# Performance work log

Measured on AMD Instinct MI355X. Metric: run time of the kernel, lower is better.

The kernel has to match this reference:

```python
import jax, jax.numpy as jnp
import numpy as np

N = 50000      # nodes
E = 800000     # edges (avg degree 16)
IN = 128       # in_feats
HID = 32       # hidden_feats per head
H = 4          # num_heads
NEG_SLOPE = 0.2


def setup_inputs() -> dict:
    key = jax.random.key(0)
    ks = jax.random.split(key, 13)
    x = jax.random.normal(ks[0], (N, IN), jnp.float32)
    src = jax.random.randint(ks[1], (E,), 0, N, jnp.int32)
    dst = jax.random.randint(ks[2], (E,), 0, N, jnp.int32)

    def lin(k, fi, fo):
        return jax.random.normal(k, (fi, fo), jnp.float32) * (1.0 / np.sqrt(fi))

    # conv1: IN -> H*HID
    W1 = lin(ks[3], IN, H * HID)
    al1 = jax.random.normal(ks[4], (H, HID), jnp.float32) * 0.1
    ar1 = jax.random.normal(ks[5], (H, HID), jnp.float32) * 0.1
    b1 = jnp.zeros((H, HID), jnp.float32)
    # conv2: H*HID -> H*HID
    W2 = lin(ks[6], H * HID, H * HID)
    al2 = jax.random.normal(ks[7], (H, HID), jnp.float32) * 0.1
    ar2 = jax.random.normal(ks[8], (H, HID), jnp.float32) * 0.1
    b2 = jnp.zeros((H, HID), jnp.float32)
    # fc: HID -> 1
    fcW = lin(ks[9], HID, 1)
    fcb = jnp.zeros((1,), jnp.float32)
    return {"x": x, "src": src, "dst": dst,
            "W1": W1, "al1": al1, "ar1": ar1, "b1": b1,
            "W2": W2, "al2": al2, "ar2": ar2, "b2": b2,
            "fcW": fcW, "fcb": fcb}


def gat_conv(x, src, dst, W, al, ar, b):
    # x: [N, F_in] -> feat: [N, H, HID]
    feat = (x @ W).reshape(N, H, HID)
    el = jnp.sum(feat * al, axis=-1)            # [N, H]
    er = jnp.sum(feat * ar, axis=-1)            # [N, H]
    e = jax.nn.leaky_relu(el[src] + er[dst], NEG_SLOPE)  # [E, H]
    # segment softmax over incoming edges of each dst node
    m = jax.ops.segment_max(e, dst, num_segments=N)      # [N, H]
    ex = jnp.exp(e - m[dst])                              # [E, H]
    denom = jax.ops.segment_sum(ex, dst, num_segments=N)  # [N, H]
    alpha = ex / denom[dst]                                # [E, H]
    msg = feat[src] * alpha[:, :, None]                    # [E, H, HID]
    out = jax.ops.segment_sum(msg, dst, num_segments=N)   # [N, H, HID]
    return out + b[None, :, :]


def reference(x, src, dst, W1, al1, ar1, b1, W2, al2, ar2, b2, fcW, fcb):
    h = gat_conv(x, src, dst, W1, al1, ar1, b1).reshape(N, H * HID)
    h = jax.nn.relu(h)
    # dropout(0.5) is identity in eval mode
    h = gat_conv(h, src, dst, W2, al2, ar2, b2).mean(axis=1)  # [N, HID]
    return h @ fcW + fcb                                       # [N, 1]
```

## Files before the change

### kernel.cpp

```cpp
#include <hip/hip_runtime.h>
#include <hip/hip_fp16.h>

#define LEAK 0.2f
#define CAP 64
#define CS 16

static __device__ inline int swz(int c, int j) {
    int qb = j >> 3, r = j & 7;
    return c * 144 + qb * 8 + (qb >> 2) * 4 + r;
}
static __device__ inline unsigned q4(float4 v, float is) {
    int x0 = __float2int_rn(v.x * is) + 128; x0 = min(max(x0, 0), 255);
    int x1 = __float2int_rn(v.y * is) + 128; x1 = min(max(x1, 0), 255);
    int x2 = __float2int_rn(v.z * is) + 128; x2 = min(max(x2, 0), 255);
    int x3 = __float2int_rn(v.w * is) + 128; x3 = min(max(x3, 0), 255);
    return (unsigned)x0 | ((unsigned)x1 << 8) | ((unsigned)x2 << 16) | ((unsigned)x3 << 24);
}

__global__ __launch_bounds__(256) void k0(
    int* __restrict__ cnt,
    const float* __restrict__ W2, const float* __restrict__ al2,
    const float* __restrict__ ar2, const float* __restrict__ fcW,
    const float* __restrict__ b2, float* __restrict__ WfT,
    float* __restrict__ bc, int N, int zb) {
    const int b = blockIdx.x;
    const int t = threadIdx.x;
    if (b < zb) {
        int i = b * 256 + t;
        if (i < N * (CS / 4)) ((int4*)cnt)[i] = make_int4(0, 0, 0, 0);
        return;
    }
    int idx = (b - zb) * 256 + t;
    if (idx < 1536) {
        int c = idx >> 7, k = idx & 127;
        int h = c & 3, sel = c >> 2;
        const float* vec = (sel == 0) ? (al2 + 32 * h)
                         : (sel == 1) ? (ar2 + 32 * h) : fcW;
        float s = 0.f;
#pragma unroll 8
        for (int m = 0; m < 32; m++) s += W2[k * 128 + 32 * h + m] * vec[m];
        WfT[c * 128 + k] = s;
    } else if (idx < 1540) {
        int h = idx - 1536;
        float s = 0.f;
        for (int m = 0; m < 32; m++) s += b2[h * 32 + m] * fcW[m];
        bc[h] = s;
    }
}

__global__ __launch_bounds__(256, 4) void k1f(
    const float* __restrict__ X, const float* __restrict__ W,
    const float* __restrict__ al, const float* __restrict__ ar,
    float2* __restrict__ elsc2, float* __restrict__ er_nh,
    unsigned* __restrict__ fq8,
    const int* __restrict__ src, const int* __restrict__ dst,
    int* __restrict__ cnt, unsigned short* __restrict__ ell,
    int N, int E, int gtiles, int R) {
    __shared__ float sW[32 * 128];
    __shared__ float sXT[32 * 64];
    const int b = blockIdx.x;
    const int t = threadIdx.x;

    if (b >= gtiles) {
        const int bb = b - gtiles;
        const int part = bb & 7;
        const int rank = bb >> 3;
        const int S = (N + 7) >> 3;
        const int lo = part * S;
        const int hi = (lo + S < N) ? (lo + S) : N;
        const int per = (E + R - 1) / R;
        const int e0 = rank * per;
        const int e1 = (e0 + per < E) ? (e0 + per) : E;
        for (int e = e0 + t; e < e1; e += 256) {
            int d = dst[e];
            if (d >= lo && d < hi) {
                int s = src[e];
                int pos = atomicAdd(&cnt[d * CS], 1);
                if (pos < CAP) ell[(size_t)d * CAP + pos] = (unsigned short)s;
            }
        }
        return;
    }

    const int r0 = b * 64;
    const int tx = t & 15;
    const int ty = t >> 4;
    const float4* X4 = (const float4*)X;
    const float4* W4 = (const float4*)W;
    float4* sW4 = (float4*)sW;
    const float4* sXT4 = (const float4*)sXT;

    float4 acc[4][2];
#pragma unroll
    for (int r = 0; r < 4; r++) {
        acc[r][0] = make_float4(0.f, 0.f, 0.f, 0.f);
        acc[r][1] = make_float4(0.f, 0.f, 0.f, 0.f);
    }
    for (int ks = 0; ks < 4; ++ks) {
        if (ks) __syncthreads();
#pragma unroll
        for (int i = 0; i < 4; i++) {
            int idx = i * 256 + t;
            sW4[idx] = W4[1024 * ks + idx];
        }
#pragma unroll
        for (int i = 0; i < 2; i++) {
            int idx = i * 256 + t;
            int row = idx >> 3;
            int kq = idx & 7;
            float4 v = make_float4(0.f, 0.f, 0.f, 0.f);
            if (r0 + row < N) v = X4[(size_t)(r0 + row) * 32 + ks * 8 + kq];
            int sc = ((row >> 2) ^ kq) * 4 + (row & 3);
            sXT[(4 * kq + 0) * 64 + sc] = v.x;
            sXT[(4 * kq + 1) * 64 + sc] = v.y;
            sXT[(4 * kq + 2) * 64 + sc] = v.z;
            sXT[(4 * kq + 3) * 64 + sc] = v.w;
        }
        __syncthreads();
#pragma unroll 4
        for (int k = 0; k < 32; k++) {
            float4 w0 = sW4[k * 32 + tx];
            float4 w1 = sW4[k * 32 + 16 + tx];
            float4 x0 = sXT4[k * 16 + (ty ^ (k >> 2))];
            float xs[4] = {x0.x, x0.y, x0.z, x0.w};
#pragma unroll
            for (int r = 0; r < 4; r++) {
                acc[r][0].x += xs[r] * w0.x; acc[r][0].y += xs[r] * w0.y;
                acc[r][0].z += xs[r] * w0.z; acc[r][0].w += xs[r] * w0.w;
                acc[r][1].x += xs[r] * w1.x; acc[r][1].y += xs[r] * w1.y;
                acc[r][1].z += xs[r] * w1.z; acc[r][1].w += xs[r] * w1.w;
            }
        }
    }
    const float4* al4p = (const float4*)al;
    const float4* ar4p = (const float4*)ar;
    float4 alA = al4p[tx], alB = al4p[16 + tx];
    float4 arA = ar4p[tx], arB = ar4p[16 + tx];
#pragma unroll
    for (int r = 0; r < 4; r++) {
        int row = r0 + ty * 4 + r;
        bool ok = row < N;
        float4 a0 = acc[r][0], a1 = acc[r][1];
        float m = fmaxf(fmaxf(fmaxf(fabsf(a0.x), fabsf(a0.y)),
                              fmaxf(fabsf(a0.z), fabsf(a0.w))),
                        fmaxf(fmaxf(fabsf(a1.x), fabsf(a1.y)),
                              fmaxf(fabsf(a1.z), fabsf(a1.w))));
#pragma unroll
        for (int off = 1; off < 16; off <<= 1) m = fmaxf(m, __shfl_xor(m, off));
        float scale = m * (1.f / 127.f);
        float is = (m > 0.f) ? (127.f / m) : 0.f;
        if (ok) {
            fq8[(size_t)row * 32 + tx] = q4(a0, is);
            fq8[(size_t)row * 32 + 16 + tx] = q4(a1, is);
        }
        float elA = a0.x * alA.x + a0.y * alA.y + a0.z * alA.z + a0.w * alA.w;
        float erA = a0.x * arA.x + a0.y * arA.y + a0.z * arA.z + a0.w * arA.w;
        float elB = a1.x * alB.x + a1.y * alB.y + a1.z * alB.z + a1.w * alB.w;
        float erB = a1.x * arB.x + a1.y * arB.y + a1.z * arB.z + a1.w * arB.w;
#pragma unroll
        for (int off = 1; off < 8; off <<= 1) {
            elA += __shfl_xor(elA, off); erA += __shfl_xor(erA, off);
            elB += __shfl_xor(elB, off); erB += __shfl_xor(erB, off);
        }
        if (ok && tx == 0) {
            elsc2[row * 4 + 0] = make_float2(elA, scale);
            elsc2[row * 4 + 2] = make_float2(elB, scale);
            er_nh[row * 4 + 0] = erA;
            er_nh[row * 4 + 2] = erB;
        }
        if (ok && tx == 8) {
            elsc2[row * 4 + 1] = make_float2(elA, scale);
            elsc2[row * 4 + 3] = make_float2(elB, scale);
            er_nh[row * 4 + 1] = erA;
            er_nh[row * 4 + 3] = erB;
        }
    }
}

__global__ __launch_bounds__(256) void k_agg1P(
    const unsigned* __restrict__ fq8, const float2* __restrict__ elsc2,
    const float* __restrict__ er_nh, const unsigned short* __restrict__ ell,
    const int* __restrict__ cnt, const float* __restrict__ b1,
    const float* __restrict__ WfT, float2* __restrict__ Pag,
    float* __restrict__ er2, int N) {
    __shared__ float sWf[12 * 144];
    for (int i = threadIdx.x; i < 1536; i += 256)
        sWf[swz(i >> 7, i & 127)] = WfT[i];
    __syncthreads();
    const int wave = threadIdx.x >> 6, lane = threadIdx.x & 63;
    const int nsub = lane >> 4, q = lane & 15, h = q >> 2;
    const int wbase = q * 8 + (q >> 2) * 4;
    const uint2* fq2 = (const uint2*)fq8;

    const int n = blockIdx.x * 16 + wave * 4 + nsub;
    const bool nok = n < N;
    const int nc = nok ? n : (N - 1);
    int deg = nok ? cnt[n * CS] : 0; if (deg > CAP) deg = CAP;
    float er = nok ? er_nh[n * 4 + h] : 0.f;
    const unsigned short* row = ell + (size_t)nc * CAP;

    int dm = deg;
    dm = max(dm, __shfl_xor(dm, 16));
    dm = max(dm, __shfl_xor(dm, 32));

    float acc[8] = {0.f, 0.f, 0.f, 0.f, 0.f, 0.f, 0.f, 0.f};
    float den = 0.f, wss = 0.f;
    for (int jt = 0; jt < dm; jt += 16) {
        int s_all = (jt + q < CAP) ? (int)row[jt + q] : 0;
        int lim = dm - jt; if (lim > 16) lim = 16;
        for (int u = 0; u < lim; u += 8) {
            int sv[8]; float2 esv[8]; uint2 fv[8];
#pragma unroll
            for (int v = 0; v < 8; v++) {
                int jj = jt + u + v;
                int s = __shfl(s_all, (lane & 48) | ((u + v) & 15));
                sv[v] = (jj < deg) ? s : 0;
            }
#pragma unroll
            for (int v = 0; v < 8; v++) esv[v] = elsc2[sv[v] * 4 + h];
#pragma unroll
            for (int v = 0; v < 8; v++) fv[v] = fq2[(size_t)sv[v] * 16 + q];
#pragma unroll
            for (int v = 0; v < 8; v++) {
                int jj = jt + u + v;
                bool valid = jj < deg;
                float e = esv[v].x + er;
                e = fmaxf(e, LEAK * e);
                float w = valid ? __expf(e) : 0.f;
                float ws = w * esv[v].y;
                unsigned ua = fv[v].x, ub = fv[v].y;
                acc[0] += ws * (float)(ua & 0xff);
                acc[1] += ws * (float)((ua >> 8) & 0xff);
                acc[2] += ws * (float)((ua >> 16) & 0xff);
                acc[3] += ws * (float)(ua >> 24);
                acc[4] += ws * (float)(ub & 0xff);
                acc[5] += ws * (float)((ub >> 8) & 0xff);
                acc[6] += ws * (float)((ub >> 16) & 0xff);
                acc[7] += ws * (float)(ub >> 24);
                den += w; wss += ws;
            }
        }
    }
    float inv = (den > 0.f) ? (1.f / den) : 0.f;
    float off128 = 128.f * wss;
    float4 b1a = ((const float4*)b1)[q * 2];
    float4 b1b = ((const float4*)b1)[q * 2 + 1];
    float hv[8];
    hv[0] = fmaxf((acc[0] - off128) * inv + b1a.x, 0.f);
    hv[1] = fmaxf((acc[1] - off128) * inv + b1a.y, 0.f);
    hv[2] = fmaxf((acc[2] - off128) * inv + b1a.z, 0.f);
    hv[3] = fmaxf((acc[3] - off128) * inv + b1a.w, 0.f);
    hv[4] = fmaxf((acc[4] - off128) * inv + b1b.x, 0.f);
    hv[5] = fmaxf((acc[5] - off128) * inv + b1b.y, 0.f);
    hv[6] = fmaxf((acc[6] - off128) * inv + b1b.z, 0.f);
    hv[7] = fmaxf((acc[7] - off128) * inv + b1b.w, 0.f);
    float p[12];
#pragma unroll
    for (int c = 0; c < 12; c++) {
        const float* wr = sWf + c * 144 + wbase;
        float4 wa = *(const float4*)wr;
        float4 wb = *(const float4*)(wr + 4);
        p[c] = hv[0] * wa.x + hv[1] * wa.y + hv[2] * wa.z + hv[3] * wa.w
             + hv[4] * wb.x + hv[5] * wb.y + hv[6] * wb.z + hv[7] * wb.w;
    }
#pragma unroll
    for (int off = 1; off < 16; off <<= 1) {
#pragma unroll
        for (int c = 0; c < 12; c++) p[c] += __shfl_xor(p[c], off);
    }
    if (nok) {
        if (q < 4) Pag[(size_t)n * 4 + q] = make_float2(p[q], p[8 + q]);
        else if (q < 8) er2[(size_t)n * 4 + (q - 4)] = p[q];
    }
}

__global__ __launch_bounds__(256) void k_agg2(
    const float2* __restrict__ Pag, const float* __restrict__ er2,
    const unsigned short* __restrict__ ell, const int* __restrict__ cnt,
    const float* __restrict__ bc, const float* __restrict__ fcb,
    float* __restrict__ out, int N) {
    int idx = blockIdx.x * 256 + threadIdx.x;
    int n = idx >> 2, h = idx & 3;
    if (n >= N) return;
    int deg = cnt[n * CS]; if (deg > CAP) deg = CAP;
    float er = er2[(size_t)n * 4 + h];
    const unsigned short* row = ell + (size_t)n * CAP;
    float num = 0.f, den = 0.f;
    int j = 0, d8 = deg & ~7;
    for (; j < d8; j += 8) {
        ushort4 sa = *(const ushort4*)(row + j);
        ushort4 sb = *(const ushort4*)(row + j + 4);
        int sv[8] = {sa.x, sa.y, sa.z, sa.w, sb.x, sb.y, sb.z, sb.w};
        float2 g[8];
#pragma unroll
        for (int v = 0; v < 8; v++) g[v] = Pag[(size_t)sv[v] * 4 + h];
#pragma unroll
        for (int v = 0; v < 8; v++) {
            float e = g[v].x + er; e = fmaxf(e, LEAK * e);
            float w = __expf(e);
            num += w * g[v].y; den += w;
        }
    }
    for (; j < deg; ++j) {
        int s = row[j];
        float2 gg = Pag[(size_t)s * 4 + h];
        float e = gg.x + er; e = fmaxf(e, LEAK * e);
        float w = __expf(e);
        num += w * gg.y; den += w;
    }
    float r = (den > 0.f) ? (num / den) : 0.f;
    r += bc[h];
    r += __shfl_xor(r, 1);
    r += __shfl_xor(r, 2);
    if (h == 0) out[n] = 0.25f * r + fcb[0];
}

extern "C" void kernel_launch(void* const* d_in, const int* in_sizes, int n_in,
                              void* d_out, int out_size, void* d_ws, size_t ws_size,
                              hipStream_t stream) {
    const float* x   = (const float*)d_in[0];
    const int* src   = (const int*)d_in[1];
    const int* dst   = (const int*)d_in[2];
    const float* W1  = (const float*)d_in[3];
    const float* al1 = (const float*)d_in[4];
    const float* ar1 = (const float*)d_in[5];
    const float* b1  = (const float*)d_in[6];
    const float* W2  = (const float*)d_in[7];
    const float* al2 = (const float*)d_in[8];
    const float* ar2 = (const float*)d_in[9];
    const float* b2  = (const float*)d_in[10];
    const float* fcW = (const float*)d_in[11];
    const float* fcb = (const float*)d_in[12];
    float* out = (float*)d_out;

    const int N = in_sizes[0] / 128;
    const int E = in_sizes[1];

    char* w = (char*)d_ws;
    size_t off = 0;
    auto alloc = [&](size_t bytes) {
        void* p = w + off;
        off = (off + bytes + 255) & ~(size_t)255;
        return p;
    };
    unsigned* fq8  = (unsigned*)alloc((size_t)N * 32 * 4);
    float2* elsc2  = (float2*)alloc((size_t)N * 4 * 8);
    float* er_nh   = (float*)alloc((size_t)N * 4 * 4);
    float2* Pag    = (float2*)alloc((size_t)N * 4 * 8);
    float* er2     = (float*)alloc((size_t)N * 4 * 4);
    float* WfT     = (float*)alloc((size_t)(12 * 128 + 4) * 4);
    float* bc      = WfT + 12 * 128;
    int* cnt       = (int*)alloc((size_t)N * CS * 4);
    unsigned short* ell = (unsigned short*)alloc((size_t)N * CAP * 2);

    const int zb = (N * (CS / 4) + 255) / 256;
    const int gtiles = (N + 63) / 64;
    const int R = 256;

    k0<<<zb + 7, 256, 0, stream>>>(
        cnt, W2, al2, ar2, fcW, b2, WfT, bc, N, zb);
    k1f<<<gtiles + 8 * R, 256, 0, stream>>>(
        x, W1, al1, ar1, elsc2, er_nh, fq8,
        src, dst, cnt, ell, N, E, gtiles, R);
    k_agg1P<<<(N + 15) / 16, 256, 0, stream>>>(
        fq8, elsc2, er_nh, ell, cnt, b1, WfT, Pag, er2, N);
    k_agg2<<<(N * 4 + 255) / 256, 256, 0, stream>>>(
        Pag, er2, ell, cnt, bc, fcb, out, N);
}
```

Baseline: 189.9 us.

## Split ELL edge-bucketing into separate kernel from projection GEMM

Moves the edge-to-ELL bucketing out of the fused projection kernel into its own kernel, k_ell. In the old scheme 8 partition blocks each rescanned the full edge list and kept only the edges whose destination fell in their node range. The new kernel reads each edge once, four edges per thread, and does the atomic insert directly. This removes the 8x redundant reads of src/dst but gives up running the scatter alongside the GEMM. It adds an extra launch, and atomics now hit random destinations across all nodes instead of a partitioned subset.

```diff
diff --git a/kernel.cpp b/kernel.cpp
--- a/kernel.cpp
+++ b/kernel.cpp
@@ -48,41 +48,35 @@
     }
 }
 
-__global__ __launch_bounds__(256, 4) void k1f(
+__global__ __launch_bounds__(256) void k_ell(
+    const int* __restrict__ src, const int* __restrict__ dst,
+    int* __restrict__ cnt, unsigned short* __restrict__ ell, int E) {
+    const int i0 = blockIdx.x * 1024 + threadIdx.x;
+    int d[4], s[4];
+#pragma unroll
+    for (int u = 0; u < 4; u++) {
+        int e = i0 + u * 256;
+        d[u] = (e < E) ? dst[e] : -1;
+        s[u] = (e < E) ? src[e] : 0;
+    }
+#pragma unroll
+    for (int u = 0; u < 4; u++) {
+        if (d[u] >= 0) {
+            int pos = atomicAdd(&cnt[d[u] * CS], 1);
+            if (pos < CAP) ell[(size_t)d[u] * CAP + pos] = (unsigned short)s[u];
+        }
+    }
+}
+
+__global__ __launch_bounds__(256, 4) void k1g(
     const float* __restrict__ X, const float* __restrict__ W,
     const float* __restrict__ al, const float* __restrict__ ar,
     float2* __restrict__ elsc2, float* __restrict__ er_nh,
-    unsigned* __restrict__ fq8,
-    const int* __restrict__ src, const int* __restrict__ dst,
-    int* __restrict__ cnt, unsigned short* __restrict__ ell,
-    int N, int E, int gtiles, int R) {
+    unsigned* __restrict__ fq8, int N) {
     __shared__ float sW[32 * 128];
     __shared__ float sXT[32 * 64];
-    const int b = blockIdx.x;
     const int t = threadIdx.x;
-
-    if (b >= gtiles) {
-        const int bb = b - gtiles;
-        const int part = bb & 7;
-        const int rank = bb >> 3;
-        const int S = (N + 7) >> 3;
-        const int lo = part * S;
-        const int hi = (lo + S < N) ? (lo + S) : N;
-        const int per = (E + R - 1) / R;
-        const int e0 = rank * per;
-        const int e1 = (e0 + per < E) ? (e0 + per) : E;
-        for (int e = e0 + t; e < e1; e += 256) {
-            int d = dst[e];
-            if (d >= lo && d < hi) {
-                int s = src[e];
-                int pos = atomicAdd(&cnt[d * CS], 1);
-                if (pos < CAP) ell[(size_t)d * CAP + pos] = (unsigned short)s;
-            }
-        }
-        return;
-    }
-
-    const int r0 = b * 64;
+    const int r0 = blockIdx.x * 64;
     const int tx = t & 15;
     const int ty = t >> 4;
     const float4* X4 = (const float4*)X;
@@ -355,13 +349,12 @@
 
     const int zb = (N * (CS / 4) + 255) / 256;
     const int gtiles = (N + 63) / 64;
-    const int R = 256;
 
     k0<<<zb + 7, 256, 0, stream>>>(
         cnt, W2, al2, ar2, fcW, b2, WfT, bc, N, zb);
-    k1f<<<gtiles + 8 * R, 256, 0, stream>>>(
-        x, W1, al1, ar1, elsc2, er_nh, fq8,
-        src, dst, cnt, ell, N, E, gtiles, R);
+    k_ell<<<(E + 1023) / 1024, 256, 0, stream>>>(src, dst, cnt, ell, E);
+    k1g<<<gtiles, 256, 0, stream>>>(
+        x, W1, al1, ar1, elsc2, er_nh, fq8, N);
     k_agg1P<<<(N + 15) / 16, 256, 0, stream>>>(
         fq8, elsc2, er_nh, ell, cnt, b1, WfT, Pag, er2, N);
     k_agg2<<<(N * 4 + 255) / 256, 256, 0, stream>>>(
```

New measurement: 219.4 us. 15.5% more time.

## Split ELL build into separate kernel with 4x unrolled dst loads

Applied to the files above, without the earlier changes.

The fused kernel that handled both the feature GEMM tiles and the ELL adjacency build is split into two kernels: k_ell for the adjacency scatter and k1g for the projection. The ELL loop now loads four dst values per iteration so more memory requests are in flight, and it reads src only for edges that pass the range check. The ELL blocks no longer carry the GEMM kernel's shared-memory footprint or occupancy limit. The trade-off is an extra launch and the two phases no longer running concurrently on the same stream.

```diff
diff --git a/kernel.cpp b/kernel.cpp
--- a/kernel.cpp
+++ b/kernel.cpp
@@ -48,41 +48,57 @@
     }
 }
 
-__global__ __launch_bounds__(256, 4) void k1f(
+__global__ __launch_bounds__(256) void k_ell(
+    const int* __restrict__ src, const int* __restrict__ dst,
+    int* __restrict__ cnt, unsigned short* __restrict__ ell,
+    int E, int N, int R) {
+    const int part = blockIdx.x & 7;
+    const int rank = blockIdx.x >> 3;
+    const int S = (N + 7) >> 3;
+    const int lo = part * S;
+    const int hi = (lo + S < N) ? (lo + S) : N;
+    const int per = (E + R - 1) / R;
+    const int e0 = rank * per;
+    const int e1 = (e0 + per < E) ? (e0 + per) : E;
+    int e = e0 + threadIdx.x;
+    for (; e + 768 < e1; e += 1024) {
+        int d0 = dst[e];       int d1 = dst[e + 256];
+        int d2 = dst[e + 512]; int d3 = dst[e + 768];
+        if (d0 >= lo && d0 < hi) {
+            int pos = atomicAdd(&cnt[d0 * CS], 1);
+            if (pos < CAP) ell[(size_t)d0 * CAP + pos] = (unsigned short)src[e];
+        }
+        if (d1 >= lo && d1 < hi) {
+            int pos = atomicAdd(&cnt[d1 * CS], 1);
+            if (pos < CAP) ell[(size_t)d1 * CAP + pos] = (unsigned short)src[e + 256];
+        }
+        if (d2 >= lo && d2 < hi) {
+            int pos = atomicAdd(&cnt[d2 * CS], 1);
+            if (pos < CAP) ell[(size_t)d2 * CAP + pos] = (unsigned short)src[e + 512];
+        }
+        if (d3 >= lo && d3 < hi) {
+            int pos = atomicAdd(&cnt[d3 * CS], 1);
+            if (pos < CAP) ell[(size_t)d3 * CAP + pos] = (unsigned short)src[e + 768];
+        }
+    }
+    for (; e < e1; e += 256) {
+        int d = dst[e];
+        if (d >= lo && d < hi) {
+            int pos = atomicAdd(&cnt[d * CS], 1);
+            if (pos < CAP) ell[(size_t)d * CAP + pos] = (unsigned short)src[e];
+        }
+    }
+}
+
+__global__ __launch_bounds__(256, 4) void k1g(
     const float* __restrict__ X, const float* __restrict__ W,
     const float* __restrict__ al, const float* __restrict__ ar,
     float2* __restrict__ elsc2, float* __restrict__ er_nh,
-    unsigned* __restrict__ fq8,
-    const int* __restrict__ src, const int* __restrict__ dst,
-    int* __restrict__ cnt, unsigned short* __restrict__ ell,
-    int N, int E, int gtiles, int R) {
+    unsigned* __restrict__ fq8, int N) {
     __shared__ float sW[32 * 128];
     __shared__ float sXT[32 * 64];
-    const int b = blockIdx.x;
     const int t = threadIdx.x;
-
-    if (b >= gtiles) {
-        const int bb = b - gtiles;
-        const int part = bb & 7;
-        const int rank = bb >> 3;
-        const int S = (N + 7) >> 3;
-        const int lo = part * S;
-        const int hi = (lo + S < N) ? (lo + S) : N;
-        const int per = (E + R - 1) / R;
-        const int e0 = rank * per;
-        const int e1 = (e0 + per < E) ? (e0 + per) : E;
-        for (int e = e0 + t; e < e1; e += 256) {
-            int d = dst[e];
-            if (d >= lo && d < hi) {
-                int s = src[e];
-                int pos = atomicAdd(&cnt[d * CS], 1);
-                if (pos < CAP) ell[(size_t)d * CAP + pos] = (unsigned short)s;
-            }
-        }
-        return;
-    }
-
-    const int r0 = b * 64;
+    const int r0 = blockIdx.x * 64;
     const int tx = t & 15;
     const int ty = t >> 4;
     const float4* X4 = (const float4*)X;
@@ -359,9 +375,9 @@
 
     k0<<<zb + 7, 256, 0, stream>>>(
         cnt, W2, al2, ar2, fcW, b2, WfT, bc, N, zb);
-    k1f<<<gtiles + 8 * R, 256, 0, stream>>>(
-        x, W1, al1, ar1, elsc2, er_nh, fq8,
-        src, dst, cnt, ell, N, E, gtiles, R);
+    k_ell<<<8 * R, 256, 0, stream>>>(src, dst, cnt, ell, E, N, R);
+    k1g<<<gtiles, 256, 0, stream>>>(
+        x, W1, al1, ar1, elsc2, er_nh, fq8, N);
     k_agg1P<<<(N + 15) / 16, 256, 0, stream>>>(
         fq8, elsc2, er_nh, ell, cnt, b1, WfT, Pag, er2, N);
     k_agg2<<<(N * 4 + 255) / 256, 256, 0, stream>>>(
```

Measured after the change: 200.0 us. +5.3%, slower.
